# Kernel tuning notes

Hardware: AMD Instinct MI355X
Metric: run time of the kernel (lower is better)

## Reference

```python
import jax, jax.numpy as jnp
import numpy as np
from jax import lax

B, T, H = 64, 1024, 256
MAX_DUR = 3            # durations drawn in [0, 4)
OUT_LEN = T * MAX_DUR  # static upper bound on expanded length


def setup_inputs() -> dict:
    key = jax.random.key(0)
    ks = jax.random.split(key, 8)
    s_conv = 1.0 / np.sqrt(H * 3)
    s_lin = 1.0 / np.sqrt(H)
    return {
        "x": jax.random.normal(ks[0], (B, T, H), dtype=jnp.float32),
        "target_durations": jax.random.randint(ks[1], (B, T), 0, MAX_DUR + 1),
        "conv1_w": jax.random.uniform(ks[2], (H, H, 3), jnp.float32, -s_conv, s_conv),
        "conv1_b": jax.random.uniform(ks[3], (H,), jnp.float32, -s_conv, s_conv),
        "conv2_w": jax.random.uniform(ks[4], (H, H, 3), jnp.float32, -s_conv, s_conv),
        "conv2_b": jax.random.uniform(ks[5], (H,), jnp.float32, -s_conv, s_conv),
        "proj_w": jax.random.uniform(ks[6], (H, 1), jnp.float32, -s_lin, s_lin),
        "proj_b": jax.random.uniform(ks[7], (1,), jnp.float32, -s_lin, s_lin),
    }


def _conv1d(x, w, b):
    # x: [B, T, C]; w: [O, I, K]; SAME padding, conv over time axis
    y = lax.conv_general_dilated(
        jnp.transpose(x, (0, 2, 1)), w, window_strides=(1,), padding="SAME",
        dimension_numbers=("NCH", "OIH", "NCH"))
    return jnp.transpose(y, (0, 2, 1)) + b


def _length_regulator(x, durations):
    # gather-based repeat_interleave: cumsum of durations + searchsorted index map
    cum = jnp.cumsum(durations, axis=1)                      # [B, T]
    pos = jnp.arange(OUT_LEN)                                # [OUT]
    idx = jax.vmap(lambda c: jnp.searchsorted(c, pos, side="right"))(cum)  # [B, OUT]
    mask = pos[None, :] < cum[:, -1][:, None]                # valid output frames
    idx = jnp.minimum(idx, T - 1)
    out = jnp.take_along_axis(x, idx[..., None], axis=1)     # [B, OUT, H]
    return out * mask[..., None].astype(x.dtype)


def reference(x, target_durations, conv1_w, conv1_b, conv2_w, conv2_b, proj_w, proj_b):
    # duration predictor (dropout = identity in eval)
    h = jax.nn.relu(_conv1d(x, conv1_w, conv1_b))
    h = jax.nn.relu(_conv1d(h, conv2_w, conv2_b))
    log_duration_prediction = (h @ proj_w + proj_b)[..., 0]  # [B, T]
    # training path: use ground-truth durations
    output = _length_regulator(x, target_durations)
    return output, log_duration_prediction
```

## Files before the change

### kernel.cpp

```cpp
#include <hip/hip_runtime.h>
#include <hip/hip_bf16.h>

#define B_  64
#define T_  1024
#define H_  256
#define OUT_LEN_ 3072

typedef __attribute__((ext_vector_type(8))) short short8v;
typedef __attribute__((ext_vector_type(4))) float floatx4;

__device__ __forceinline__ unsigned short f2bf_rne(float f) {
    unsigned int u = __float_as_uint(f);
    u += 0x7FFFu + ((u >> 16) & 1u);
    return (unsigned short)(u >> 16);
}
__device__ __forceinline__ float bf2f(unsigned short h) {
    return __uint_as_float(((unsigned int)h) << 16);
}

__device__ __forceinline__ void gload_lds16(const void* g, void* l) {
    __builtin_amdgcn_global_load_lds(
        (const __attribute__((address_space(1))) unsigned int*)g,
        (__attribute__((address_space(3))) unsigned int*)l, 16, 0, 0);
}

__global__ __launch_bounds__(256) void convert_w_kernel(
    const float* __restrict__ w, unsigned short* __restrict__ wq)
{
    int e = blockIdx.x * 256 + threadIdx.x;
    if (e >= H_ * H_ * 3) return;
    int o = e / (H_ * 3);
    int rem = e - o * (H_ * 3);
    int ic = rem / 3;
    int tap = rem - ic * 3;
    float v = w[e];
    unsigned short h = f2bf_rne(v);
    unsigned short l = f2bf_rne(v - bf2f(h));
    int c = ic >> 5, grp = (ic >> 3) & 3, el = ic & 7;
    size_t hi_idx = ((((size_t)(c * 2 + 0) * 3 + tap) * 4 + grp) * 256 + o) * 8 + el;
    size_t lo_idx = ((((size_t)(c * 2 + 1) * 3 + tap) * 4 + grp) * 256 + o) * 8 + el;
    wq[hi_idx] = h;
    wq[lo_idx] = l;
}

__global__ __launch_bounds__(256) void init_ld_kernel(float* __restrict__ ld,
                                                      const float* __restrict__ pb) {
    int i = blockIdx.x * 256 + threadIdx.x;
    if (i < B_ * T_) ld[i] = pb[0];
}

template <int MODE>
__global__ __launch_bounds__(256, 2) void conv_mfma_kernel(
    const float* __restrict__ xin,
    const unsigned int* __restrict__ pin,
    const unsigned short* __restrict__ wq,
    const float* __restrict__ bias,
    const float* __restrict__ pw,
    unsigned int* __restrict__ opacked,
    float* __restrict__ logdur)
{
    __shared__ __align__(16) char lds[69952];
    char* XsH = lds;
    char* XsL = lds + 10400;
    char* Ws  = lds + 20800;

    const int tid  = threadIdx.x;
    const int t0   = blockIdx.x * 128;
    const int o0   = blockIdx.y * 128;
    const int b    = blockIdx.z;
    const int lane = tid & 63;
    const int wave = tid >> 6;
    const int r    = lane & 15;
    const int g    = lane >> 4;
    const int wm   = wave >> 1;
    const int wn   = wave & 1;

    const size_t abase = (size_t)b * T_ * H_;

    floatx4 acc[4][4];
    #pragma unroll
    for (int fn = 0; fn < 4; ++fn) {
        float bv = bias[o0 + wn * 64 + fn * 16 + r];
        #pragma unroll
        for (int fm = 0; fm < 4; ++fm)
            acc[fm][fn] = (floatx4){bv, bv, bv, bv};
    }

    for (int ic0 = 0; ic0 < H_; ic0 += 32) {
        __syncthreads();
        {
            const unsigned short* wqc = wq + (size_t)(ic0 >> 5) * 49152;
            #pragma unroll
            for (int it = 0; it < 12; ++it) {
                int wl = wave * 12 + it;
                int half = wl & 1;
                int atg = wl >> 1;
                const unsigned short* src =
                    wqc + ((size_t)atg * 256 + o0 + half * 64 + lane) * 8;
                char* dst = Ws + (size_t)(atg * 128 + half * 64) * 16;
                gload_lds16(src, dst);
            }
        }
        for (int p = tid; p < 520; p += 256) {
            int row = p >> 2, grp = p & 3;
            int gt = t0 - 1 + row;
            short8v hv = {0, 0, 0, 0, 0, 0, 0, 0};
            short8v lv = {0, 0, 0, 0, 0, 0, 0, 0};
            if (gt >= 0 && gt < T_) {
                if constexpr (MODE == 0) {
                    const float4* s =
                        (const float4*)(xin + abase + (size_t)gt * H_ + ic0 + grp * 8);
                    float4 a = s[0], c = s[1];
                    float vv[8] = {a.x, a.y, a.z, a.w, c.x, c.y, c.z, c.w};
                    #pragma unroll
                    for (int j = 0; j < 8; ++j) {
                        unsigned short h = f2bf_rne(vv[j]);
                        hv[j] = (short)h;
                        lv[j] = (short)f2bf_rne(vv[j] - bf2f(h));
                    }
                } else {
                    const uint4* s =
                        (const uint4*)(pin + abase + (size_t)gt * H_ + ic0 + grp * 8);
                    uint4 a = s[0], c = s[1];
                    unsigned int uu[8] = {a.x, a.y, a.z, a.w, c.x, c.y, c.z, c.w};
                    #pragma unroll
                    for (int j = 0; j < 8; ++j) {
                        hv[j] = (short)(uu[j] & 0xffffu);
                        lv[j] = (short)(uu[j] >> 16);
                    }
                }
            }
            int off = row * 80 + grp * 16;
            *(short8v*)(XsH + off) = hv;
            *(short8v*)(XsL + off) = lv;
        }
        __syncthreads();

        #pragma unroll
        for (int tap = 0; tap < 3; ++tap) {
            short8v aH[4], aL[4], bH[4], bL[4];
            #pragma unroll
            for (int fm = 0; fm < 4; ++fm) {
                int off = (wm * 64 + fm * 16 + r + tap) * 80 + g * 16;
                aH[fm] = *(const short8v*)(XsH + off);
                aL[fm] = *(const short8v*)(XsL + off);
            }
            #pragma unroll
            for (int fn = 0; fn < 4; ++fn) {
                int ocl = wn * 64 + fn * 16 + r;
                bH[fn] = *(const short8v*)(Ws + (size_t)(((0 * 3 + tap) * 4 + g) * 128 + ocl) * 16);
                bL[fn] = *(const short8v*)(Ws + (size_t)(((1 * 3 + tap) * 4 + g) * 128 + ocl) * 16);
            }
            #pragma unroll
            for (int fm = 0; fm < 4; ++fm)
                #pragma unroll
                for (int fn = 0; fn < 4; ++fn) {
                    acc[fm][fn] = __builtin_amdgcn_mfma_f32_16x16x32_bf16(
                        aH[fm], bH[fn], acc[fm][fn], 0, 0, 0);
                    acc[fm][fn] = __builtin_amdgcn_mfma_f32_16x16x32_bf16(
                        aH[fm], bL[fn], acc[fm][fn], 0, 0, 0);
                    acc[fm][fn] = __builtin_amdgcn_mfma_f32_16x16x32_bf16(
                        aL[fm], bH[fn], acc[fm][fn], 0, 0, 0);
                }
        }
    }

    if constexpr (MODE == 0) {
        unsigned int* ob = opacked + abase;
        #pragma unroll
        for (int fm = 0; fm < 4; ++fm) {
            int trow = t0 + wm * 64 + fm * 16 + g * 4;
            #pragma unroll
            for (int fn = 0; fn < 4; ++fn) {
                int o = o0 + wn * 64 + fn * 16 + r;
                #pragma unroll
                for (int reg = 0; reg < 4; ++reg) {
                    float v = fmaxf(acc[fm][fn][reg], 0.f);
                    unsigned short h = f2bf_rne(v);
                    unsigned short l = f2bf_rne(v - bf2f(h));
                    ob[(size_t)(trow + reg) * H_ + o] =
                        (unsigned int)h | ((unsigned int)l << 16);
                }
            }
        }
    } else {
        float pwv[4];
        #pragma unroll
        for (int fn = 0; fn < 4; ++fn) pwv[fn] = pw[o0 + wn * 64 + fn * 16 + r];
        #pragma unroll
        for (int fm = 0; fm < 4; ++fm) {
            #pragma unroll
            for (int reg = 0; reg < 4; ++reg) {
                float s = 0.f;
                #pragma unroll
                for (int fn = 0; fn < 4; ++fn)
                    s += fmaxf(acc[fm][fn][reg], 0.f) * pwv[fn];
                s += __shfl_xor(s, 1, 64);
                s += __shfl_xor(s, 2, 64);
                s += __shfl_xor(s, 4, 64);
                s += __shfl_xor(s, 8, 64);
                if (r == 0)
                    atomicAdd(&logdur[(size_t)b * T_ + t0 + wm * 64 + fm * 16 + g * 4 + reg], s);
            }
        }
    }
}

__global__ __launch_bounds__(256) void regulator_kernel(
    const float* __restrict__ x, const int* __restrict__ dur,
    float* __restrict__ out)
{
    const int b  = blockIdx.y;
    const int r0 = blockIdx.x * 128;
    const int tid = threadIdx.x;
    const int lane = tid & 63;
    const int wv = tid >> 6;

    __shared__ int cum[T_];
    __shared__ int wtot[4];
    __shared__ int sidx[128];

    const int* drow = dur + (size_t)b * T_;
    int base = tid * 4;
    int d0 = drow[base + 0], d1 = drow[base + 1], d2 = drow[base + 2], d3 = drow[base + 3];
    int i0 = d0, i1 = i0 + d1, i2 = i1 + d2, i3 = i2 + d3;
    int lt = i3;
    int v = lt;
    #pragma unroll
    for (int delta = 1; delta < 64; delta <<= 1) {
        int u = __shfl_up(v, delta, 64);
        if (lane >= delta) v += u;
    }
    if (lane == 63) wtot[wv] = v;
    __syncthreads();
    int woff = 0;
    #pragma unroll
    for (int i = 0; i < 4; ++i)
        if (i < wv) woff += wtot[i];
    int excl = woff + v - lt;
    cum[base + 0] = excl + i0;
    cum[base + 1] = excl + i1;
    cum[base + 2] = excl + i2;
    cum[base + 3] = excl + i3;
    __syncthreads();

    int tot = cum[T_ - 1];
    if (tid < 128) {
        int p = r0 + tid;
        int lo = 0, hi = T_;
        while (lo < hi) {
            int mid = (lo + hi) >> 1;
            if (cum[mid] <= p) lo = mid + 1; else hi = mid;
        }
        int idx = lo > (T_ - 1) ? (T_ - 1) : lo;
        sidx[tid] = (p < tot) ? idx : -1;
    }
    __syncthreads();

    const float4* x4 = (const float4*)(x + (size_t)b * T_ * H_);
    float4* o4 = (float4*)(out + ((size_t)b * OUT_LEN_ + r0) * H_);
    for (int rr = 0; rr < 128; rr += 4) {
        int rw = rr + wv;
        int idx = sidx[rw];
        float4 val;
        if (idx >= 0) val = x4[(size_t)idx * (H_ / 4) + lane];
        else          val = make_float4(0.f, 0.f, 0.f, 0.f);
        o4[(size_t)rw * (H_ / 4) + lane] = val;
    }
}

extern "C" void kernel_launch(void* const* d_in, const int* in_sizes, int n_in,
                              void* d_out, int out_size, void* d_ws, size_t ws_size,
                              hipStream_t stream) {
    const float* x   = (const float*)d_in[0];
    const int*   dur = (const int*)d_in[1];
    const float* w1  = (const float*)d_in[2];
    const float* b1  = (const float*)d_in[3];
    const float* w2  = (const float*)d_in[4];
    const float* b2  = (const float*)d_in[5];
    const float* pw  = (const float*)d_in[6];
    const float* pb  = (const float*)d_in[7];

    float* out = (float*)d_out;
    char*  p   = (char*)d_out;

    unsigned int*   h1p = (unsigned int*)(p);
    unsigned short* wq1 = (unsigned short*)(p + 134217728u);
    unsigned short* wq2 = (unsigned short*)(p + 135004160u);
    float* logdur = out + (size_t)B_ * OUT_LEN_ * H_;

    convert_w_kernel<<<768, 256, 0, stream>>>(w1, wq1);
    convert_w_kernel<<<768, 256, 0, stream>>>(w2, wq2);
    init_ld_kernel<<<(B_ * T_) / 256, 256, 0, stream>>>(logdur, pb);

    dim3 cgrid(T_ / 128, H_ / 128, B_);
    conv_mfma_kernel<0><<<cgrid, 256, 0, stream>>>(
        x, nullptr, wq1, b1, nullptr, h1p, nullptr);
    conv_mfma_kernel<1><<<cgrid, 256, 0, stream>>>(
        nullptr, h1p, wq2, b2, pw, nullptr, logdur);

    regulator_kernel<<<dim3(OUT_LEN_ / 128, B_), 256, 0, stream>>>(x, dur, out);
}
```

Before: 397.4 us.

## Double-buffer activation tiles and read conv weights directly from global memory

```diff
diff --git a/kernel.cpp b/kernel.cpp
--- a/kernel.cpp
+++ b/kernel.cpp
@@ -16,12 +16,6 @@
 }
 __device__ __forceinline__ float bf2f(unsigned short h) {
     return __uint_as_float(((unsigned int)h) << 16);
-}
-
-__device__ __forceinline__ void gload_lds16(const void* g, void* l) {
-    __builtin_amdgcn_global_load_lds(
-        (const __attribute__((address_space(1))) unsigned int*)g,
-        (__attribute__((address_space(3))) unsigned int*)l, 16, 0, 0);
 }
 
 __global__ __launch_bounds__(256) void convert_w_kernel(
@@ -59,10 +53,7 @@
     unsigned int* __restrict__ opacked,
     float* __restrict__ logdur)
 {
-    __shared__ __align__(16) char lds[69952];
-    char* XsH = lds;
-    char* XsL = lds + 10400;
-    char* Ws  = lds + 20800;
+    __shared__ __align__(16) char lds[2][20800];
 
     const int tid  = threadIdx.x;
     const int t0   = blockIdx.x * 128;
@@ -77,6 +68,16 @@
 
     const size_t abase = (size_t)b * T_ * H_;
 
+    const int srow0 = tid >> 2, sgrp = tid & 3;
+    const int gt0 = t0 - 1 + srow0;
+    const int gt1 = gt0 + 64;
+    const int gt2 = t0 - 1 + 128 + (tid >> 2);
+    const bool v0 = (gt0 >= 0) && (gt0 < T_);
+    const bool v1 = (gt1 < T_);
+    const bool v2 = (tid < 8) && (gt2 < T_);
+
+    const unsigned short* wb = wq + (size_t)g * 2048 + (size_t)(o0 + wn * 64 + r) * 8;
+
     floatx4 acc[4][4];
     #pragma unroll
     for (int fn = 0; fn < 4; ++fn) {
@@ -86,70 +87,119 @@
             acc[fm][fn] = (floatx4){bv, bv, bv, bv};
     }
 
-    for (int ic0 = 0; ic0 < H_; ic0 += 32) {
-        __syncthreads();
-        {
-            const unsigned short* wqc = wq + (size_t)(ic0 >> 5) * 49152;
-            #pragma unroll
-            for (int it = 0; it < 12; ++it) {
-                int wl = wave * 12 + it;
-                int half = wl & 1;
-                int atg = wl >> 1;
-                const unsigned short* src =
-                    wqc + ((size_t)atg * 256 + o0 + half * 64 + lane) * 8;
-                char* dst = Ws + (size_t)(atg * 128 + half * 64) * 16;
-                gload_lds16(src, dst);
-            }
-        }
-        for (int p = tid; p < 520; p += 256) {
-            int row = p >> 2, grp = p & 3;
-            int gt = t0 - 1 + row;
-            short8v hv = {0, 0, 0, 0, 0, 0, 0, 0};
-            short8v lv = {0, 0, 0, 0, 0, 0, 0, 0};
-            if (gt >= 0 && gt < T_) {
-                if constexpr (MODE == 0) {
-                    const float4* s =
-                        (const float4*)(xin + abase + (size_t)gt * H_ + ic0 + grp * 8);
-                    float4 a = s[0], c = s[1];
-                    float vv[8] = {a.x, a.y, a.z, a.w, c.x, c.y, c.z, c.w};
-                    #pragma unroll
-                    for (int j = 0; j < 8; ++j) {
-                        unsigned short h = f2bf_rne(vv[j]);
-                        hv[j] = (short)h;
-                        lv[j] = (short)f2bf_rne(vv[j] - bf2f(h));
-                    }
-                } else {
-                    const uint4* s =
-                        (const uint4*)(pin + abase + (size_t)gt * H_ + ic0 + grp * 8);
-                    uint4 a = s[0], c = s[1];
-                    unsigned int uu[8] = {a.x, a.y, a.z, a.w, c.x, c.y, c.z, c.w};
-                    #pragma unroll
-                    for (int j = 0; j < 8; ++j) {
-                        hv[j] = (short)(uu[j] & 0xffffu);
-                        lv[j] = (short)(uu[j] >> 16);
-                    }
-                }
-            }
-            int off = row * 80 + grp * 16;
-            *(short8v*)(XsH + off) = hv;
-            *(short8v*)(XsL + off) = lv;
-        }
-        __syncthreads();
-
+    auto stage_commit = [&](int buf, short8v h0, short8v l0, short8v h1,
+                            short8v l1, short8v h2, short8v l2) {
+        char* XsH = lds[buf];
+        char* XsL = lds[buf] + 10400;
+        int off0 = srow0 * 80 + sgrp * 16;
+        *(short8v*)(XsH + off0) = h0;
+        *(short8v*)(XsL + off0) = l0;
+        int off1 = off0 + 64 * 80;
+        *(short8v*)(XsH + off1) = h1;
+        *(short8v*)(XsL + off1) = l1;
+        if (tid < 8) {
+            int off2 = (128 + (tid >> 2)) * 80 + sgrp * 16;
+            *(short8v*)(XsH + off2) = h2;
+            *(short8v*)(XsL + off2) = l2;
+        }
+    };
+
+    #define LOAD_X_F32(gt, valid, ra, rb)                                        \
+        if (valid) {                                                             \
+            const float4* s = (const float4*)(xin + abase + (size_t)(gt) * H_ +  \
+                                              ic_n + sgrp * 8);                  \
+            ra = s[0]; rb = s[1];                                                \
+        }
+    #define LOAD_X_U32(gt, valid, ra, rb)                                        \
+        if (valid) {                                                             \
+            const uint4* s = (const uint4*)(pin + abase + (size_t)(gt) * H_ +    \
+                                            ic_n + sgrp * 8);                    \
+            ra = s[0]; rb = s[1];                                                \
+        }
+    #define CVT_F32(ra, rb, hv, lv)                                              \
+        {                                                                        \
+            float vv[8] = {ra.x, ra.y, ra.z, ra.w, rb.x, rb.y, rb.z, rb.w};      \
+            _Pragma("unroll")                                                    \
+            for (int j = 0; j < 8; ++j) {                                        \
+                unsigned short h = f2bf_rne(vv[j]);                              \
+                hv[j] = (short)h;                                                \
+                lv[j] = (short)f2bf_rne(vv[j] - bf2f(h));                        \
+            }                                                                    \
+        }
+    #define CVT_U32(ra, rb, hv, lv)                                              \
+        {                                                                        \
+            unsigned int uu[8] = {ra.x, ra.y, ra.z, ra.w, rb.x, rb.y, rb.z, rb.w};\
+            _Pragma("unroll")                                                    \
+            for (int j = 0; j < 8; ++j) {                                        \
+                hv[j] = (short)(uu[j] & 0xffffu);                                \
+                lv[j] = (short)(uu[j] >> 16);                                    \
+            }                                                                    \
+        }
+
+    {
+        const int ic_n = 0;
+        float4 fa0{}, fb0{}, fa1{}, fb1{}, fa2{}, fb2{};
+        uint4  ua0{}, ub0{}, ua1{}, ub1{}, ua2{}, ub2{};
+        if constexpr (MODE == 0) {
+            LOAD_X_F32(gt0, v0, fa0, fb0);
+            LOAD_X_F32(gt1, v1, fa1, fb1);
+            LOAD_X_F32(gt2, v2, fa2, fb2);
+        } else {
+            LOAD_X_U32(gt0, v0, ua0, ub0);
+            LOAD_X_U32(gt1, v1, ua1, ub1);
+            LOAD_X_U32(gt2, v2, ua2, ub2);
+        }
+        short8v h0{}, l0{}, h1{}, l1{}, h2{}, l2{};
+        if constexpr (MODE == 0) {
+            CVT_F32(fa0, fb0, h0, l0);
+            CVT_F32(fa1, fb1, h1, l1);
+            CVT_F32(fa2, fb2, h2, l2);
+        } else {
+            CVT_U32(ua0, ub0, h0, l0);
+            CVT_U32(ua1, ub1, h1, l1);
+            CVT_U32(ua2, ub2, h2, l2);
+        }
+        stage_commit(0, h0, l0, h1, l1, h2, l2);
+    }
+    __syncthreads();
+
+    #pragma unroll 2
+    for (int c = 0; c < 8; ++c) {
+        const int cur = c & 1;
+        const bool pf = (c < 7);
+        const int ic_n = (c + 1) * 32;
+
+        float4 fa0{}, fb0{}, fa1{}, fb1{}, fa2{}, fb2{};
+        uint4  ua0{}, ub0{}, ua1{}, ub1{}, ua2{}, ub2{};
+        if (pf) {
+            if constexpr (MODE == 0) {
+                LOAD_X_F32(gt0, v0, fa0, fb0);
+                LOAD_X_F32(gt1, v1, fa1, fb1);
+                LOAD_X_F32(gt2, v2, fa2, fb2);
+            } else {
+                LOAD_X_U32(gt0, v0, ua0, ub0);
+                LOAD_X_U32(gt1, v1, ua1, ub1);
+                LOAD_X_U32(gt2, v2, ua2, ub2);
+            }
+        }
+
+        const char* XsH = lds[cur];
+        const char* XsL = lds[cur] + 10400;
+        const unsigned short* wc = wb + (size_t)c * 24 * 2048;
+        const int arow = (wm * 64 + r) * 80 + g * 16;
         #pragma unroll
         for (int tap = 0; tap < 3; ++tap) {
             short8v aH[4], aL[4], bH[4], bL[4];
             #pragma unroll
+            for (int fn = 0; fn < 4; ++fn) {
+                bH[fn] = *(const short8v*)(wc + (size_t)tap * 4 * 2048 + fn * 128);
+                bL[fn] = *(const short8v*)(wc + (size_t)(12 + tap * 4) * 2048 + fn * 128);
+            }
+            #pragma unroll
             for (int fm = 0; fm < 4; ++fm) {
-                int off = (wm * 64 + fm * 16 + r + tap) * 80 + g * 16;
+                int off = arow + (fm * 16 + tap) * 80;
                 aH[fm] = *(const short8v*)(XsH + off);
                 aL[fm] = *(const short8v*)(XsL + off);
-            }
-            #pragma unroll
-            for (int fn = 0; fn < 4; ++fn) {
-                int ocl = wn * 64 + fn * 16 + r;
-                bH[fn] = *(const short8v*)(Ws + (size_t)(((0 * 3 + tap) * 4 + g) * 128 + ocl) * 16);
-                bL[fn] = *(const short8v*)(Ws + (size_t)(((1 * 3 + tap) * 4 + g) * 128 + ocl) * 16);
             }
             #pragma unroll
             for (int fm = 0; fm < 4; ++fm)
@@ -163,6 +213,21 @@
                         aL[fm], bH[fn], acc[fm][fn], 0, 0, 0);
                 }
         }
+
+        if (pf) {
+            short8v h0{}, l0{}, h1{}, l1{}, h2{}, l2{};
+            if constexpr (MODE == 0) {
+                CVT_F32(fa0, fb0, h0, l0);
+                CVT_F32(fa1, fb1, h1, l1);
+                CVT_F32(fa2, fb2, h2, l2);
+            } else {
+                CVT_U32(ua0, ub0, h0, l0);
+                CVT_U32(ua1, ub1, h1, l1);
+                CVT_U32(ua2, ub2, h2, l2);
+            }
+            stage_commit(cur ^ 1, h0, l0, h1, l1, h2, l2);
+        }
+        __syncthreads();
     }
 
     if constexpr (MODE == 0) {
```

After: 397.2 us. No clear change (-0.0%).

## Pre-split activations into padded bf16 planes and double-buffer conv LDS staging

Applied to the files above, without the earlier changes.

```diff
diff --git a/kernel.cpp b/kernel.cpp
--- a/kernel.cpp
+++ b/kernel.cpp
@@ -5,6 +5,7 @@
 #define T_  1024
 #define H_  256
 #define OUT_LEN_ 3072
+#define TP_ 1056
 
 typedef __attribute__((ext_vector_type(8))) short short8v;
 typedef __attribute__((ext_vector_type(4))) float floatx4;
@@ -17,7 +18,11 @@
 __device__ __forceinline__ float bf2f(unsigned short h) {
     return __uint_as_float(((unsigned int)h) << 16);
 }
-
+__device__ __forceinline__ unsigned int packhl(float v) {
+    unsigned short h = f2bf_rne(v);
+    unsigned short l = f2bf_rne(v - bf2f(h));
+    return (unsigned int)h | ((unsigned int)l << 16);
+}
 __device__ __forceinline__ void gload_lds16(const void* g, void* l) {
     __builtin_amdgcn_global_load_lds(
         (const __attribute__((address_space(1))) unsigned int*)g,
@@ -43,6 +48,45 @@
     wq[lo_idx] = l;
 }
 
+__global__ __launch_bounds__(256) void convert_x_kernel(
+    const float* __restrict__ x, unsigned short* __restrict__ xh,
+    unsigned short* __restrict__ xl)
+{
+    int gid = blockIdx.x * 256 + threadIdx.x;
+    int b = gid >> 15;
+    int rem = gid & 32767;
+    int t = rem >> 5;
+    int gp = rem & 31;
+    const float4* s = (const float4*)(x + ((size_t)b * T_ + t) * H_ + gp * 8);
+    float4 a = s[0], c = s[1];
+    float vv[8] = {a.x, a.y, a.z, a.w, c.x, c.y, c.z, c.w};
+    short8v hv, lv;
+    #pragma unroll
+    for (int j = 0; j < 8; ++j) {
+        unsigned short h = f2bf_rne(vv[j]);
+        hv[j] = (short)h;
+        lv[j] = (short)f2bf_rne(vv[j] - bf2f(h));
+    }
+    size_t d = ((size_t)b * TP_ + t + 1) * H_ + gp * 8;
+    *(short8v*)(xh + d) = hv;
+    *(short8v*)(xl + d) = lv;
+}
+
+__global__ __launch_bounds__(256) void zero_pads_kernel(
+    unsigned short* p0, unsigned short* p1, unsigned short* p2, unsigned short* p3)
+{
+    int gid = blockIdx.x * 256 + threadIdx.x;
+    unsigned short* planes[4] = {p0, p1, p2, p3};
+    int pl = gid >> 16;
+    int rem = gid & 65535;
+    int b = rem >> 10;
+    int rr = (rem >> 5) & 31;
+    int gp = rem & 31;
+    int row = (rr == 0) ? 0 : (1024 + rr);
+    short8v z = {0, 0, 0, 0, 0, 0, 0, 0};
+    *(short8v*)(planes[pl] + ((size_t)b * TP_ + row) * H_ + gp * 8) = z;
+}
+
 __global__ __launch_bounds__(256) void init_ld_kernel(float* __restrict__ ld,
                                                       const float* __restrict__ pb) {
     int i = blockIdx.x * 256 + threadIdx.x;
@@ -50,32 +94,29 @@
 }
 
 template <int MODE>
-__global__ __launch_bounds__(256, 2) void conv_mfma_kernel(
-    const float* __restrict__ xin,
-    const unsigned int* __restrict__ pin,
+__global__ __launch_bounds__(256, 3) void conv_mfma_kernel(
+    const unsigned short* __restrict__ xh, const unsigned short* __restrict__ xl,
     const unsigned short* __restrict__ wq,
-    const float* __restrict__ bias,
-    const float* __restrict__ pw,
-    unsigned int* __restrict__ opacked,
+    const float* __restrict__ bias, const float* __restrict__ pw,
+    unsigned short* __restrict__ oh, unsigned short* __restrict__ olo,
     float* __restrict__ logdur)
 {
-    __shared__ __align__(16) char lds[69952];
-    char* XsH = lds;
-    char* XsL = lds + 10400;
-    char* Ws  = lds + 20800;
-
-    const int tid  = threadIdx.x;
-    const int t0   = blockIdx.x * 128;
-    const int o0   = blockIdx.y * 128;
-    const int b    = blockIdx.z;
+    __shared__ __align__(16) char lds[40960];
+
+    const int tid = threadIdx.x;
+    const int t0 = blockIdx.x * 128;
+    const int o0 = blockIdx.y * 128;
+    const int b  = blockIdx.z;
     const int lane = tid & 63;
     const int wave = tid >> 6;
-    const int r    = lane & 15;
-    const int g    = lane >> 4;
-    const int wm   = wave >> 1;
-    const int wn   = wave & 1;
-
-    const size_t abase = (size_t)b * T_ * H_;
+    const int r = lane & 15, g = lane >> 4;
+    const int wm = wave >> 1, wn = wave & 1;
+
+    const unsigned short* splane = (wm == 0) ? xh : xl;
+    const size_t srow0 = (size_t)b * TP_ + t0 + wn * 80;
+    const int lrow = lane >> 2, lgrp = lane & 3;
+
+    const unsigned short* wb = wq + (size_t)g * 2048 + (size_t)(o0 + wn * 64 + r) * 8;
 
     floatx4 acc[4][4];
     #pragma unroll
@@ -86,71 +127,40 @@
             acc[fm][fn] = (floatx4){bv, bv, bv, bv};
     }
 
-    for (int ic0 = 0; ic0 < H_; ic0 += 32) {
-        __syncthreads();
-        {
-            const unsigned short* wqc = wq + (size_t)(ic0 >> 5) * 49152;
-            #pragma unroll
-            for (int it = 0; it < 12; ++it) {
-                int wl = wave * 12 + it;
-                int half = wl & 1;
-                int atg = wl >> 1;
-                const unsigned short* src =
-                    wqc + ((size_t)atg * 256 + o0 + half * 64 + lane) * 8;
-                char* dst = Ws + (size_t)(atg * 128 + half * 64) * 16;
-                gload_lds16(src, dst);
-            }
-        }
-        for (int p = tid; p < 520; p += 256) {
-            int row = p >> 2, grp = p & 3;
-            int gt = t0 - 1 + row;
-            short8v hv = {0, 0, 0, 0, 0, 0, 0, 0};
-            short8v lv = {0, 0, 0, 0, 0, 0, 0, 0};
-            if (gt >= 0 && gt < T_) {
-                if constexpr (MODE == 0) {
-                    const float4* s =
-                        (const float4*)(xin + abase + (size_t)gt * H_ + ic0 + grp * 8);
-                    float4 a = s[0], c = s[1];
-                    float vv[8] = {a.x, a.y, a.z, a.w, c.x, c.y, c.z, c.w};
-                    #pragma unroll
-                    for (int j = 0; j < 8; ++j) {
-                        unsigned short h = f2bf_rne(vv[j]);
-                        hv[j] = (short)h;
-                        lv[j] = (short)f2bf_rne(vv[j] - bf2f(h));
-                    }
-                } else {
-                    const uint4* s =
-                        (const uint4*)(pin + abase + (size_t)gt * H_ + ic0 + grp * 8);
-                    uint4 a = s[0], c = s[1];
-                    unsigned int uu[8] = {a.x, a.y, a.z, a.w, c.x, c.y, c.z, c.w};
-                    #pragma unroll
-                    for (int j = 0; j < 8; ++j) {
-                        hv[j] = (short)(uu[j] & 0xffffu);
-                        lv[j] = (short)(uu[j] >> 16);
-                    }
-                }
-            }
-            int off = row * 80 + grp * 16;
-            *(short8v*)(XsH + off) = hv;
-            *(short8v*)(XsL + off) = lv;
-        }
-        __syncthreads();
-
+    #define STAGE(c)                                                             \
+        {                                                                        \
+            const unsigned short* sb = splane + srow0 * H_ + (c) * 32 + lgrp * 8 \
+                                       + (size_t)lrow * H_;                      \
+            char* db = lds + ((c) & 1) * 20480 + wm * 10240 + wn * 80 * 64;      \
+            _Pragma("unroll")                                                    \
+            for (int i = 0; i < 5; ++i)                                          \
+                gload_lds16(sb + (size_t)i * 16 * H_, db + i * 1024);            \
+        }
+
+    STAGE(0);
+    __syncthreads();
+
+    #pragma unroll 2
+    for (int c = 0; c < 8; ++c) {
+        if (c < 7) STAGE(c + 1);
+
+        const char* Xb = lds + (c & 1) * 20480;
+        const unsigned short* wc = wb + (size_t)c * 49152;
         #pragma unroll
         for (int tap = 0; tap < 3; ++tap) {
             short8v aH[4], aL[4], bH[4], bL[4];
             #pragma unroll
+            for (int fn = 0; fn < 4; ++fn) {
+                bH[fn] = *(const short8v*)(wc + (size_t)tap * 8192 + fn * 128);
+                bL[fn] = *(const short8v*)(wc + 24576 + (size_t)tap * 8192 + fn * 128);
+            }
+            #pragma unroll
             for (int fm = 0; fm < 4; ++fm) {
-                int off = (wm * 64 + fm * 16 + r + tap) * 80 + g * 16;
-                aH[fm] = *(const short8v*)(XsH + off);
-                aL[fm] = *(const short8v*)(XsL + off);
-            }
-            #pragma unroll
-            for (int fn = 0; fn < 4; ++fn) {
-                int ocl = wn * 64 + fn * 16 + r;
-                bH[fn] = *(const short8v*)(Ws + (size_t)(((0 * 3 + tap) * 4 + g) * 128 + ocl) * 16);
-                bL[fn] = *(const short8v*)(Ws + (size_t)(((1 * 3 + tap) * 4 + g) * 128 + ocl) * 16);
-            }
+                int off = (wm * 64 + fm * 16 + r + tap) * 64 + g * 16;
+                aH[fm] = *(const short8v*)(Xb + off);
+                aL[fm] = *(const short8v*)(Xb + 10240 + off);
+            }
+            __builtin_amdgcn_s_setprio(1);
             #pragma unroll
             for (int fm = 0; fm < 4; ++fm)
                 #pragma unroll
@@ -162,25 +172,44 @@
                     acc[fm][fn] = __builtin_amdgcn_mfma_f32_16x16x32_bf16(
                         aL[fm], bH[fn], acc[fm][fn], 0, 0, 0);
                 }
-        }
-    }
+            __builtin_amdgcn_s_setprio(0);
+        }
+        __syncthreads();
+    }
+    #undef STAGE
 
     if constexpr (MODE == 0) {
-        unsigned int* ob = opacked + abase;
-        #pragma unroll
+        unsigned int* Ltmp = (unsigned int*)lds;
+        #pragma unroll 1
         for (int fm = 0; fm < 4; ++fm) {
-            int trow = t0 + wm * 64 + fm * 16 + g * 4;
+            __syncthreads();
             #pragma unroll
             for (int fn = 0; fn < 4; ++fn) {
-                int o = o0 + wn * 64 + fn * 16 + r;
+                int ol = wn * 64 + fn * 16 + r;
+                unsigned int* wbase = Ltmp + (wm * 16 + g * 4) * 132 + ol;
                 #pragma unroll
-                for (int reg = 0; reg < 4; ++reg) {
-                    float v = fmaxf(acc[fm][fn][reg], 0.f);
-                    unsigned short h = f2bf_rne(v);
-                    unsigned short l = f2bf_rne(v - bf2f(h));
-                    ob[(size_t)(trow + reg) * H_ + o] =
-                        (unsigned int)h | ((unsigned int)l << 16);
+                for (int reg = 0; reg < 4; ++reg)
+                    wbase[reg * 132] = packhl(fmaxf(acc[fm][fn][reg], 0.f));
+            }
+            __syncthreads();
+            int tau = tid >> 3;
+            int c2 = tid & 7;
+            int gt = t0 + (tau >> 4) * 64 + fm * 16 + (tau & 15) + 1;
+            size_t dbase = ((size_t)b * TP_ + gt) * H_ + o0;
+            #pragma unroll
+            for (int half = 0; half < 2; ++half) {
+                int oc = c2 * 16 + half * 8;
+                uint4 q0 = *(const uint4*)(Ltmp + tau * 132 + oc);
+                uint4 q1 = *(const uint4*)(Ltmp + tau * 132 + oc + 4);
+                unsigned int uu[8] = {q0.x, q0.y, q0.z, q0.w, q1.x, q1.y, q1.z, q1.w};
+                short8v hv, lv;
+                #pragma unroll
+                for (int j = 0; j < 8; ++j) {
+                    hv[j] = (short)(uu[j] & 0xffffu);
+                    lv[j] = (short)(uu[j] >> 16);
                 }
+                *(short8v*)(oh + dbase + oc) = hv;
+                *(short8v*)(olo + dbase + oc) = lv;
             }
         }
     } else {
@@ -284,20 +313,25 @@
     float* out = (float*)d_out;
     char*  p   = (char*)d_out;
 
-    unsigned int*   h1p = (unsigned int*)(p);
-    unsigned short* wq1 = (unsigned short*)(p + 134217728u);
-    unsigned short* wq2 = (unsigned short*)(p + 135004160u);
+    unsigned short* xph  = (unsigned short*)(p);
+    unsigned short* xpl  = (unsigned short*)(p + 34603008u);
+    unsigned short* h1h  = (unsigned short*)(p + 69206016u);
+    unsigned short* h1l  = (unsigned short*)(p + 103809024u);
+    unsigned short* wq1  = (unsigned short*)(p + 138412032u);
+    unsigned short* wq2  = (unsigned short*)(p + 139198464u);
     float* logdur = out + (size_t)B_ * OUT_LEN_ * H_;
 
     convert_w_kernel<<<768, 256, 0, stream>>>(w1, wq1);
     convert_w_kernel<<<768, 256, 0, stream>>>(w2, wq2);
+    zero_pads_kernel<<<1024, 256, 0, stream>>>(xph, xpl, h1h, h1l);
+    convert_x_kernel<<<8192, 256, 0, stream>>>(x, xph, xpl);
     init_ld_kernel<<<(B_ * T_) / 256, 256, 0, stream>>>(logdur, pb);
 
     dim3 cgrid(T_ / 128, H_ / 128, B_);
     conv_mfma_kernel<0><<<cgrid, 256, 0, stream>>>(
-        x, nullptr, wq1, b1, nullptr, h1p, nullptr);
+        xph, xpl, wq1, b1, nullptr, h1h, h1l, nullptr);
     conv_mfma_kernel<1><<<cgrid, 256, 0, stream>>>(
-        nullptr, h1p, wq2, b2, pw, nullptr, logdur);
+        h1h, h1l, wq2, b2, pw, nullptr, nullptr, logdur);
 
     regulator_kernel<<<dim3(OUT_LEN_ / 128, B_), 256, 0, stream>>>(x, dur, out);
 }
```

After: 503.2 us. 1.27x slower.
